# Kernel optimization log

Hardware: AMD Instinct MI355X
Metric: run time of the kernel (lower is better)

Reference implementation:

```python
import jax, jax.numpy as jnp
import numpy as np

B, L, D_MODEL, H = 4, 2048, 1024, 16
HD = D_MODEL // H  # head_dim = 64


def _rope_tables(seq_len, dim, dtype):
    inv_freq = 1.0 / (10000.0 ** (jnp.arange(0, dim, 2, dtype=jnp.float32) / dim))
    t = jnp.arange(seq_len, dtype=jnp.float32)
    freqs = jnp.outer(t, inv_freq)  # (S, dim/2)
    return jnp.cos(freqs).astype(dtype), jnp.sin(freqs).astype(dtype)


def _apply_rope(x):
    # x: (B, H, S, d)
    cos, sin = _rope_tables(x.shape[-2], x.shape[-1], x.dtype)  # (S, d/2)
    x_even = x[..., 0::2]
    x_odd = x[..., 1::2]
    out_even = x_even * cos - x_odd * sin
    out_odd = x_even * sin + x_odd * cos
    return jnp.stack([out_even, out_odd], axis=-1).reshape(x.shape)


def setup_inputs() -> dict:
    key = jax.random.key(0)
    ks = jax.random.split(key, 9)
    s = 1.0 / np.sqrt(D_MODEL)
    inp = {
        "query": jax.random.normal(ks[0], (B, L, D_MODEL), dtype=jnp.float32),
        "Wq": jax.random.uniform(ks[1], (D_MODEL, D_MODEL), jnp.float32, -s, s),
        "bq": jax.random.uniform(ks[2], (D_MODEL,), jnp.float32, -s, s),
        "Wk": jax.random.uniform(ks[3], (D_MODEL, D_MODEL), jnp.float32, -s, s),
        "bk": jax.random.uniform(ks[4], (D_MODEL,), jnp.float32, -s, s),
        "Wv": jax.random.uniform(ks[5], (D_MODEL, D_MODEL), jnp.float32, -s, s),
        "bv": jax.random.uniform(ks[6], (D_MODEL,), jnp.float32, -s, s),
        "Wo": jax.random.uniform(ks[7], (D_MODEL, D_MODEL), jnp.float32, -s, s),
        "bo": jax.random.uniform(ks[8], (D_MODEL,), jnp.float32, -s, s),
    }
    return inp


def reference(query, Wq, bq, Wk, bk, Wv, bv, Wo, bo):
    Bq, Lq, _ = query.shape
    # projections (torch Linear: x @ W.T + b), split into heads -> (B, H, L, d)
    def proj(x, W, b):
        y = x @ W.T + b
        return y.reshape(Bq, Lq, H, HD).transpose(0, 2, 1, 3)
    q = _apply_rope(proj(query, Wq, bq))
    k = _apply_rope(proj(query, Wk, bk))
    v = proj(query, Wv, bv)
    scores = jnp.einsum("bhqd,bhkd->bhqk", q, k) / np.sqrt(HD)
    causal_mask = jnp.triu(jnp.ones((Lq, Lq), dtype=bool), k=1)
    scores = jnp.where(causal_mask[None, None, :, :], -jnp.inf, scores)
    attn = jax.nn.softmax(scores, axis=-1)
    out = jnp.einsum("bhqk,bhkd->bhqd", attn, v)
    out = out.transpose(0, 2, 1, 3).reshape(Bq, Lq, D_MODEL)
    return out @ Wo.T + bo
```

## Files before the change

### kernel.cpp

```cpp
#include <hip/hip_runtime.h>
#include <hip/hip_bf16.h>
#include <math.h>

#define L_SEQ  2048
#define DMODEL 1024
#define NHEAD  16
#define HEADD  64

typedef __attribute__((ext_vector_type(8))) short short8;
typedef __attribute__((ext_vector_type(4))) short short4v;
typedef __attribute__((ext_vector_type(4))) float f32x4;

static __device__ __forceinline__ unsigned short f2bf(float f) {
    unsigned int u = __float_as_uint(f);
    unsigned int r = (u + 0x7fffu + ((u >> 16) & 1u)) >> 16;
    return (unsigned short)r;
}

static __device__ __forceinline__ void dma16(const unsigned short* g, unsigned short* l) {
    __builtin_amdgcn_global_load_lds((const __attribute__((address_space(1))) void*)g,
                                     (__attribute__((address_space(3))) void*)l, 16, 0, 0);
}

__global__ __launch_bounds__(256) void prep(
    const float* __restrict__ query,
    const float* __restrict__ Wq, const float* __restrict__ Wk,
    const float* __restrict__ Wv, const float* __restrict__ Wo,
    unsigned short* __restrict__ xb, unsigned short* __restrict__ wdst,
    float* __restrict__ rope)
{
    int gid = blockIdx.x * 256 + threadIdx.x;
    if (gid < 2097152) {
        float4 v = reinterpret_cast<const float4*>(query)[gid];
        ushort4 o;
        o.x = f2bf(v.x); o.y = f2bf(v.y); o.z = f2bf(v.z); o.w = f2bf(v.w);
        reinterpret_cast<ushort4*>(xb)[gid] = o;
    } else if (gid < 2097152 + 1048576) {
        int i = gid - 2097152;
        int which = i >> 18;
        const float* src = which == 0 ? Wq : which == 1 ? Wk : which == 2 ? Wv : Wo;
        float4 v = reinterpret_cast<const float4*>(src)[i & 262143];
        ushort4 o;
        o.x = f2bf(v.x); o.y = f2bf(v.y); o.z = f2bf(v.z); o.w = f2bf(v.w);
        reinterpret_cast<ushort4*>(wdst)[i] = o;
    } else if (gid < 2097152 + 1048576 + 65536) {
        int i = gid - (2097152 + 1048576);
        int lpos = i >> 5, i2 = i & 31;
        float inv_f = expf(-0.28782313662425574f * (float)i2);
        float ang = (float)lpos * inv_f;
        rope[2 * i]     = cosf(ang);
        rope[2 * i + 1] = sinf(ang);
    }
}

#define BKP 32

__global__ __launch_bounds__(512, 4) void proj_qkv(
    const unsigned short* __restrict__ X,
    const unsigned short* __restrict__ Wqkv,
    const float* __restrict__ bq_,
    const float* __restrict__ bk_,
    const float* __restrict__ bv_,
    const float* __restrict__ rope,
    unsigned short* __restrict__ Qb,
    unsigned short* __restrict__ Kb,
    unsigned short* __restrict__ Vr)
{
    __shared__ unsigned short pool[36864];
    unsigned short* a_ring = pool;
    unsigned short* b_ring = pool + 12288;

    const int tid  = threadIdx.x;
    const int lane = tid & 63;
    const int w    = tid >> 6;
    const int wm   = w & 1, wn = w >> 1;
    const int quad = lane >> 4, l16 = lane & 15;

    const int orig = blockIdx.y * 12 + blockIdx.x;
    const int xcd  = orig & 7;
    const int k    = orig >> 3;
    const int by   = xcd * 8 + (k & 7);
    const int bxp  = k >> 3;
    const int m0   = by * 128;
    const int n0   = bxp * 256;

    const int sel = bxp >> 2;
    const float* bias   = sel == 0 ? bq_ : (sel == 1 ? bk_ : bv_);
    unsigned short* out = sel == 0 ? Qb  : (sel == 1 ? Kb  : Vr);

    const int st_row = lane >> 2;
    const int st_col = (((lane & 3) ^ ((lane >> 3) & 3)) << 3);
    const int rd = ((quad ^ ((l16 >> 1) & 3)) << 3);

    f32x4 acc[4][4];
#pragma unroll
    for (int i = 0; i < 4; ++i)
#pragma unroll
        for (int j = 0; j < 4; ++j) acc[i][j] = (f32x4){0.f, 0.f, 0.f, 0.f};

    const unsigned short* Xs = X    + (size_t)(m0 + w * 16 + st_row) * DMODEL + st_col;
    const unsigned short* Ws = Wqkv + (size_t)(n0 + w * 32 + st_row) * DMODEL + st_col;
    const int ldsA  = (w * 16) * BKP;
    const int ldsB0 = (w * 32) * BKP, ldsB1 = (w * 32 + 16) * BKP;

#pragma unroll
    for (int p = 0; p < 2; ++p) {
        const int kk = p * BKP;
        dma16(Xs + kk,               a_ring + p * 4096 + ldsA);
        dma16(Ws + kk,               b_ring + p * 8192 + ldsB0);
        dma16(Ws + 16 * DMODEL + kk, b_ring + p * 8192 + ldsB1);
    }
    asm volatile("s_waitcnt vmcnt(3)" ::: "memory");
    __builtin_amdgcn_s_barrier();

    for (int kt = 0; kt < 32; ++kt) {
        const int sA = (kt % 3) * 4096;
        const int sB = (kt % 3) * 8192;
        const int pA = ((kt + 2) % 3) * 4096;
        const int pB = ((kt + 2) % 3) * 8192;
        const int kk = ((kt + 2) & 31) * BKP;

        short8 af[4], bf[4];
#pragma unroll
        for (int i = 0; i < 4; ++i)
            af[i] = *reinterpret_cast<const short8*>(
                &a_ring[sA + (wm * 64 + i * 16 + l16) * BKP + rd]);
#pragma unroll
        for (int j = 0; j < 4; ++j)
            bf[j] = *reinterpret_cast<const short8*>(
                &b_ring[sB + (wn * 64 + j * 16 + l16) * BKP + rd]);
        dma16(Xs + kk,               a_ring + pA + ldsA);
        dma16(Ws + kk,               b_ring + pB + ldsB0);
        dma16(Ws + 16 * DMODEL + kk, b_ring + pB + ldsB1);
        __builtin_amdgcn_s_barrier();
        asm volatile("s_waitcnt lgkmcnt(0)" ::: "memory");
        __builtin_amdgcn_sched_barrier(0);
        __builtin_amdgcn_s_setprio(1);
#pragma unroll
        for (int i = 0; i < 4; ++i)
#pragma unroll
            for (int j = 0; j < 4; ++j)
                acc[i][j] = __builtin_amdgcn_mfma_f32_16x16x32_bf16(af[i], bf[j], acc[i][j], 0, 0, 0);
        __builtin_amdgcn_s_setprio(0);
        asm volatile("s_waitcnt vmcnt(3)" ::: "memory");
        __builtin_amdgcn_s_barrier();
    }
    asm volatile("s_waitcnt vmcnt(0)" ::: "memory");
    __builtin_amdgcn_s_barrier();

    const int b     = m0 >> 11;
    const int lpos0 = m0 & (L_SEQ - 1);
#pragma unroll
    for (int t = 0; t < 2; ++t) {
        if ((wn >> 1) == t) {
#pragma unroll
            for (int jf = 0; jf < 4; ++jf) {
                int nl = (wn & 1) * 64 + jf * 16 + l16;
                int nn = (bxp & 3) * 256 + t * 128 + nl;
                float bval = bias[nn];
                int d  = nn & (HEADD - 1);
                float sgn = (d & 1) ? 1.0f : -1.0f;
                int i2 = d >> 1;
#pragma unroll
                for (int mf = 0; mf < 4; ++mf) {
#pragma unroll
                    for (int r = 0; r < 4; ++r) {
                        int ml = wm * 64 + mf * 16 + quad * 4 + r;
                        int lpos = (m0 + ml) & (L_SEQ - 1);
                        float v = acc[mf][jf][r] + bval;
                        if (sel < 2) {
                            float p = __shfl_xor(v, 1);
                            float2 cs = *reinterpret_cast<const float2*>(&rope[(size_t)(lpos * 32 + i2) * 2]);
                            v = v * cs.x + sgn * cs.y * p;
                            if (sel == 0) v *= 0.18033688011112042f;
                        }
                        pool[(sel < 2) ? (ml * 136 + nl) : (nl * 136 + ml)] = f2bf(v);
                    }
                }
            }
        }
        asm volatile("s_waitcnt lgkmcnt(0)" ::: "memory");
        __builtin_amdgcn_s_barrier();
#pragma unroll
        for (int i = 0; i < 4; ++i) {
            int g   = i * 512 + tid;
            int row = g >> 4;
            int c8  = (g & 15) * 8;
            int4 val = *reinterpret_cast<const int4*>(&pool[row * 136 + c8]);
            size_t addr;
            if (sel < 2) {
                int n_g = (bxp & 3) * 256 + t * 128 + c8;
                int h = n_g >> 6, d = n_g & 63;
                addr = ((size_t)(b * NHEAD + h) * L_SEQ + (lpos0 + row)) * HEADD + d;
            } else {
                int n_g = (bxp & 3) * 256 + t * 128 + row;
                int h = n_g >> 6, d = n_g & 63;
                addr = ((size_t)(b * NHEAD + h) * HEADD + d) * L_SEQ + lpos0 + c8;
            }
            *reinterpret_cast<int4*>(out + addr) = val;
        }
        asm volatile("s_waitcnt lgkmcnt(0)" ::: "memory");
        __builtin_amdgcn_s_barrier();
    }
}

__global__ __launch_bounds__(256) void attn_fwd(
    const unsigned short* __restrict__ Q,
    const unsigned short* __restrict__ K,
    const unsigned short* __restrict__ Vt,
    unsigned short* __restrict__ Oa)
{
    __shared__ unsigned short k_lds[2][64 * 64];
    __shared__ unsigned short v_lds[2][64 * 64];
    const int tid  = threadIdx.x;
    const int lane = tid & 63;
    const int w    = tid >> 6;
    const int quad = lane >> 4, l16 = lane & 15;
    const int pair = blockIdx.y;
    const int bh   = blockIdx.x;
    const size_t base = (size_t)bh * L_SEQ * HEADD;
    const int b = bh >> 4, h = bh & 15;

    const int srow  = lane >> 3;
    const int sslot = lane & 7;
    const int ssw   = ((sslot ^ srow) << 3);
    const unsigned short* Ksrc = K  + base + (size_t)(w * 8 + srow) * HEADD + ssw;
    const unsigned short* Vsrc = Vt + base + (size_t)(w * 8 + srow) * L_SEQ + ssw;
    const int d0 = (w * 8) * 64;
    const int d1 = (32 + w * 8) * 64;
    const int swr = (l16 & 7);

    for (int half = 0; half < 2; ++half) {
        const int s = half ? (15 - pair) : pair;
        const int qrow0 = s * 128 + w * 16 + l16;
        const int qrow1 = qrow0 + 64;
        const int kbmax = 2 * s + 1;

        short8 qf0[2], qf1[2];
#pragma unroll
        for (int ks = 0; ks < 2; ++ks) {
            qf0[ks] = *reinterpret_cast<const short8*>(Q + base + (size_t)qrow0 * HEADD + ks * 32 + quad * 8);
            qf1[ks] = *reinterpret_cast<const short8*>(Q + base + (size_t)qrow1 * HEADD + ks * 32 + quad * 8);
        }

        f32x4 o0[4], o1[4];
#pragma unroll
        for (int nt = 0; nt < 4; ++nt) {
            o0[nt] = (f32x4){0.f, 0.f, 0.f, 0.f};
            o1[nt] = (f32x4){0.f, 0.f, 0.f, 0.f};
        }
        float lsum0 = 0.f, lsum1 = 0.f;

        dma16(Ksrc,                 &k_lds[0][d0]);
        dma16(Ksrc + 32 * HEADD,    &k_lds[0][d1]);
        dma16(Vsrc,                 &v_lds[0][d0]);
        dma16(Vsrc + 32 * L_SEQ,    &v_lds[0][d1]);
        asm volatile("s_waitcnt vmcnt(0)" ::: "memory");
        __builtin_amdgcn_s_barrier();

        int cur = 0;
        for (int kb = 0; kb <= kbmax; ++kb) {
            const int kn = (kb + 1) <= kbmax ? (kb + 1) : 0;
            const int nb = cur ^ 1;
            dma16(Ksrc + (size_t)(kn * 64) * HEADD,        &k_lds[nb][d0]);
            dma16(Ksrc + (size_t)(kn * 64 + 32) * HEADD,   &k_lds[nb][d1]);
            dma16(Vsrc + kn * 64,                          &v_lds[nb][d0]);
            dma16(Vsrc + kn * 64 + 32 * L_SEQ,             &v_lds[nb][d1]);

            f32x4 st0[4], st1[4];
#pragma unroll
            for (int nt = 0; nt < 4; ++nt) {
                st0[nt] = (f32x4){0.f, 0.f, 0.f, 0.f};
                st1[nt] = (f32x4){0.f, 0.f, 0.f, 0.f};
            }
            __builtin_amdgcn_s_setprio(1);
#pragma unroll
            for (int ks = 0; ks < 2; ++ks)
#pragma unroll
                for (int nt = 0; nt < 4; ++nt) {
                    short8 kf = *reinterpret_cast<const short8*>(
                        &k_lds[cur][(nt * 16 + l16) * 64 + (((ks * 4 + quad) ^ swr) << 3)]);
                    st0[nt] = __builtin_amdgcn_mfma_f32_16x16x32_bf16(kf, qf0[ks], st0[nt], 0, 0, 0);
                    st1[nt] = __builtin_amdgcn_mfma_f32_16x16x32_bf16(kf, qf1[ks], st1[nt], 0, 0, 0);
                }
            __builtin_amdgcn_s_setprio(0);

            if (kb >= 2 * s) {
#pragma unroll
                for (int nt = 0; nt < 4; ++nt)
#pragma unroll
                    for (int r = 0; r < 4; ++r) {
                        int seqcol = kb * 64 + nt * 16 + quad * 4 + r;
                        if (seqcol > qrow0) st0[nt][r] = -INFINITY;
                    }
            }
            if (kb == kbmax) {
#pragma unroll
                for (int nt = 0; nt < 4; ++nt)
#pragma unroll
                    for (int r = 0; r < 4; ++r) {
                        int seqcol = kb * 64 + nt * 16 + quad * 4 + r;
                        if (seqcol > qrow1) st1[nt][r] = -INFINITY;
                    }
            }

            short4v pfrag0[4], pfrag1[4];
#pragma unroll
            for (int nt = 0; nt < 4; ++nt) {
                float p0 = __builtin_amdgcn_exp2f(st0[nt][0]);
                float p1 = __builtin_amdgcn_exp2f(st0[nt][1]);
                float p2 = __builtin_amdgcn_exp2f(st0[nt][2]);
                float p3 = __builtin_amdgcn_exp2f(st0[nt][3]);
                lsum0 += (p0 + p1) + (p2 + p3);
                unsigned u0 = __float_as_uint(p0) + 0x8000u;
                unsigned u1 = __float_as_uint(p1) + 0x8000u;
                unsigned u2 = __float_as_uint(p2) + 0x8000u;
                unsigned u3 = __float_as_uint(p3) + 0x8000u;
                union { unsigned u[2]; short4v v; } pk;
                pk.u[0] = (u0 >> 16) | (u1 & 0xffff0000u);
                pk.u[1] = (u2 >> 16) | (u3 & 0xffff0000u);
                pfrag0[nt] = pk.v;

                float q0e = __builtin_amdgcn_exp2f(st1[nt][0]);
                float q1e = __builtin_amdgcn_exp2f(st1[nt][1]);
                float q2e = __builtin_amdgcn_exp2f(st1[nt][2]);
                float q3e = __builtin_amdgcn_exp2f(st1[nt][3]);
                lsum1 += (q0e + q1e) + (q2e + q3e);
                unsigned v0 = __float_as_uint(q0e) + 0x8000u;
                unsigned v1 = __float_as_uint(q1e) + 0x8000u;
                unsigned v2 = __float_as_uint(q2e) + 0x8000u;
                unsigned v3 = __float_as_uint(q3e) + 0x8000u;
                union { unsigned u[2]; short4v v; } pk1;
                pk1.u[0] = (v0 >> 16) | (v1 & 0xffff0000u);
                pk1.u[1] = (v2 >> 16) | (v3 & 0xffff0000u);
                pfrag1[nt] = pk1.v;
            }

            __builtin_amdgcn_s_setprio(1);
#pragma unroll
            for (int c = 0; c < 4; ++c)
#pragma unroll
                for (int nt2 = 0; nt2 < 4; ++nt2) {
                    short4v vf = *reinterpret_cast<const short4v*>(
                        &v_lds[cur][(nt2 * 16 + l16) * 64 +
                                    (((c * 2 + (quad >> 1)) ^ swr) << 3) + ((quad & 1) << 2)]);
                    o0[nt2] = __builtin_amdgcn_mfma_f32_16x16x16bf16_1k(pfrag0[c], vf, o0[nt2], 0, 0, 0);
                    o1[nt2] = __builtin_amdgcn_mfma_f32_16x16x16bf16_1k(pfrag1[c], vf, o1[nt2], 0, 0, 0);
                }
            __builtin_amdgcn_s_setprio(0);

            asm volatile("s_waitcnt vmcnt(0)" ::: "memory");
            __builtin_amdgcn_s_barrier();
            cur ^= 1;
        }

        lsum0 += __shfl_xor(lsum0, 16);
        lsum0 += __shfl_xor(lsum0, 32);
        lsum1 += __shfl_xor(lsum1, 16);
        lsum1 += __shfl_xor(lsum1, 32);
        float rs0[4], rs1[4];
#pragma unroll
        for (int r = 0; r < 4; ++r) {
            rs0[r] = __shfl(lsum0, quad * 4 + r);
            rs1[r] = __shfl(lsum1, quad * 4 + r);
        }
#pragma unroll
        for (int r = 0; r < 4; ++r) {
            float inv0 = 1.0f / rs0[r];
            float inv1 = 1.0f / rs1[r];
            int lg0 = s * 128 + w * 16 + quad * 4 + r;
            int lg1 = lg0 + 64;
#pragma unroll
            for (int nt = 0; nt < 4; ++nt) {
                int d = nt * 16 + l16;
                Oa[(size_t)(b * L_SEQ + lg0) * DMODEL + h * HEADD + d] = f2bf(o0[nt][r] * inv0);
                Oa[(size_t)(b * L_SEQ + lg1) * DMODEL + h * HEADD + d] = f2bf(o1[nt][r] * inv1);
            }
        }
    }
}

__global__ __launch_bounds__(256) void out_gemm(
    const unsigned short* __restrict__ X,
    const unsigned short* __restrict__ W,
    const float* __restrict__ bias,
    float* __restrict__ out)
{
    __shared__ unsigned short a_lds[3][128 * BKP];
    __shared__ unsigned short b_lds[3][128 * BKP];
    const int tid  = threadIdx.x;
    const int lane = tid & 63;
    const int w    = tid >> 6;
    const int wm   = w & 1, wn = w >> 1;
    const int quad = lane >> 4, l16 = lane & 15;

    const int orig = blockIdx.y * 8 + blockIdx.x;
    const int xcd  = orig & 7;
    const int k    = orig >> 3;
    const int m0   = (xcd * 8 + (k & 7)) * 128;
    const int n0   = (k >> 3) * 128;

    const int st_row = lane >> 2;
    const int st_col = (((lane & 3) ^ ((lane >> 3) & 3)) << 3);
    const int rd = ((quad ^ ((l16 >> 1) & 3)) << 3);

    f32x4 acc[4][4];
#pragma unroll
    for (int i = 0; i < 4; ++i)
#pragma unroll
        for (int j = 0; j < 4; ++j) acc[i][j] = (f32x4){0.f, 0.f, 0.f, 0.f};

    const unsigned short* Xs = X + (size_t)(m0 + w * 32 + st_row) * DMODEL + st_col;
    const unsigned short* Ws = W + (size_t)(n0 + w * 32 + st_row) * DMODEL + st_col;
    const int ldsA0 = (w * 32) * BKP, ldsA1 = (w * 32 + 16) * BKP;

#pragma unroll
    for (int p = 0; p < 2; ++p) {
        const int kk = p * BKP;
        dma16(Xs + kk,               &a_lds[p][ldsA0]);
        dma16(Xs + 16 * DMODEL + kk, &a_lds[p][ldsA1]);
        dma16(Ws + kk,               &b_lds[p][ldsA0]);
        dma16(Ws + 16 * DMODEL + kk, &b_lds[p][ldsA1]);
    }
    asm volatile("s_waitcnt vmcnt(4)" ::: "memory");
    __builtin_amdgcn_s_barrier();

    for (int kt = 0; kt < 32; ++kt) {
        const int slot = kt % 3;
        const int ps   = (kt + 2) % 3;
        const int kk   = ((kt + 2) & 31) * BKP;

        dma16(Xs + kk,               &a_lds[ps][ldsA0]);
        dma16(Xs + 16 * DMODEL + kk, &a_lds[ps][ldsA1]);
        dma16(Ws + kk,               &b_lds[ps][ldsA0]);
        dma16(Ws + 16 * DMODEL + kk, &b_lds[ps][ldsA1]);

        short8 af[4], bf[4];
#pragma unroll
        for (int i = 0; i < 4; ++i)
            af[i] = *reinterpret_cast<const short8*>(
                &a_lds[slot][(wm * 64 + i * 16 + l16) * BKP + rd]);
#pragma unroll
        for (int j = 0; j < 4; ++j)
            bf[j] = *reinterpret_cast<const short8*>(
                &b_lds[slot][(wn * 64 + j * 16 + l16) * BKP + rd]);
        asm volatile("s_waitcnt lgkmcnt(0)" ::: "memory");
        __builtin_amdgcn_sched_barrier(0);
        __builtin_amdgcn_s_setprio(1);
#pragma unroll
        for (int i = 0; i < 4; ++i)
#pragma unroll
            for (int j = 0; j < 4; ++j)
                acc[i][j] = __builtin_amdgcn_mfma_f32_16x16x32_bf16(af[i], bf[j], acc[i][j], 0, 0, 0);
        __builtin_amdgcn_s_setprio(0);
        asm volatile("s_waitcnt vmcnt(4)" ::: "memory");
        __builtin_amdgcn_s_barrier();
    }
    asm volatile("s_waitcnt vmcnt(0)" ::: "memory");

#pragma unroll
    for (int nt = 0; nt < 4; ++nt) {
        int n_g = n0 + wn * 64 + nt * 16 + l16;
        float bv = bias[n_g];
#pragma unroll
        for (int mt = 0; mt < 4; ++mt)
#pragma unroll
            for (int r = 0; r < 4; ++r) {
                int m_g = m0 + wm * 64 + mt * 16 + quad * 4 + r;
                out[(size_t)m_g * DMODEL + n_g] = acc[mt][nt][r] + bv;
            }
    }
}

extern "C" void kernel_launch(void* const* d_in, const int* in_sizes, int n_in,
                              void* d_out, int out_size, void* d_ws, size_t ws_size,
                              hipStream_t stream) {
    const float* query = (const float*)d_in[0];
    const float* Wq = (const float*)d_in[1];
    const float* bq = (const float*)d_in[2];
    const float* Wk = (const float*)d_in[3];
    const float* bk = (const float*)d_in[4];
    const float* Wv = (const float*)d_in[5];
    const float* bv = (const float*)d_in[6];
    const float* Wo = (const float*)d_in[7];
    const float* bo = (const float*)d_in[8];
    float* out = (float*)d_out;

    unsigned short* ws  = (unsigned short*)d_ws;
    unsigned short* xb  = ws;
    unsigned short* wqb = xb  + (size_t)8388608;
    unsigned short* wkb = wqb + 1048576;
    unsigned short* wvb = wkb + 1048576;
    unsigned short* wob = wvb + 1048576;
    unsigned short* Qb  = wob + 1048576;
    unsigned short* Kb  = Qb  + 8388608;
    unsigned short* Vr  = Kb  + 8388608;
    unsigned short* Ab  = Vr  + 8388608;
    float* rope = (float*)(Ab + 8388608);

    (void)wkb; (void)wvb;

    prep<<<12545, 256, 0, stream>>>(query, Wq, Wk, Wv, Wo, xb, wqb, rope);

    proj_qkv<<<dim3(12, 64), 512, 0, stream>>>(xb, wqb, bq, bk, bv, rope, Qb, Kb, Vr);
    attn_fwd<<<dim3(64, 8), 256, 0, stream>>>(Qb, Kb, Vr, Ab);
    out_gemm<<<dim3(8, 64), 256, 0, stream>>>(Ab, wob, bo, out);
}
```

Before: 277.6 us.

## Triple-buffer K/V tiles in attention with two-block-ahead async prefetch

Expands the K and V LDS staging from double to triple buffering and issues the global-to-LDS DMA two key blocks ahead. The wait becomes vmcnt(4), so only the older block's loads must land before each barrier, letting one block's loads stay in flight across the compute of the next. The goal is to hide global load latency in the attention loop. The cost is 50% more LDS per block, which may lower occupancy, plus modulo-3 slot indexing.

Result: faster. 267.6 us (-3.6%).

```diff
diff --git a/kernel.cpp b/kernel.cpp
--- a/kernel.cpp
+++ b/kernel.cpp
@@ -210,8 +210,8 @@
     const unsigned short* __restrict__ Vt,
     unsigned short* __restrict__ Oa)
 {
-    __shared__ unsigned short k_lds[2][64 * 64];
-    __shared__ unsigned short v_lds[2][64 * 64];
+    __shared__ unsigned short k_lds[3][64 * 64];
+    __shared__ unsigned short v_lds[3][64 * 64];
     const int tid  = threadIdx.x;
     const int lane = tid & 63;
     const int w    = tid >> 6;
@@ -251,21 +251,24 @@
         }
         float lsum0 = 0.f, lsum1 = 0.f;
 
-        dma16(Ksrc,                 &k_lds[0][d0]);
-        dma16(Ksrc + 32 * HEADD,    &k_lds[0][d1]);
-        dma16(Vsrc,                 &v_lds[0][d0]);
-        dma16(Vsrc + 32 * L_SEQ,    &v_lds[0][d1]);
-        asm volatile("s_waitcnt vmcnt(0)" ::: "memory");
-        __builtin_amdgcn_s_barrier();
-
-        int cur = 0;
+#pragma unroll
+        for (int p = 0; p < 2; ++p) {
+            dma16(Ksrc + (size_t)(p * 64) * HEADD,        &k_lds[p][d0]);
+            dma16(Ksrc + (size_t)(p * 64 + 32) * HEADD,   &k_lds[p][d1]);
+            dma16(Vsrc + p * 64,                          &v_lds[p][d0]);
+            dma16(Vsrc + p * 64 + 32 * L_SEQ,             &v_lds[p][d1]);
+        }
+        asm volatile("s_waitcnt vmcnt(4)" ::: "memory");
+        __builtin_amdgcn_s_barrier();
+
         for (int kb = 0; kb <= kbmax; ++kb) {
-            const int kn = (kb + 1) <= kbmax ? (kb + 1) : 0;
-            const int nb = cur ^ 1;
-            dma16(Ksrc + (size_t)(kn * 64) * HEADD,        &k_lds[nb][d0]);
-            dma16(Ksrc + (size_t)(kn * 64 + 32) * HEADD,   &k_lds[nb][d1]);
-            dma16(Vsrc + kn * 64,                          &v_lds[nb][d0]);
-            dma16(Vsrc + kn * 64 + 32 * L_SEQ,             &v_lds[nb][d1]);
+            const int slot = kb % 3;
+            const int ps   = (kb + 2) % 3;
+            const int kn   = (kb + 2) <= kbmax ? (kb + 2) : 0;
+            dma16(Ksrc + (size_t)(kn * 64) * HEADD,        &k_lds[ps][d0]);
+            dma16(Ksrc + (size_t)(kn * 64 + 32) * HEADD,   &k_lds[ps][d1]);
+            dma16(Vsrc + kn * 64,                          &v_lds[ps][d0]);
+            dma16(Vsrc + kn * 64 + 32 * L_SEQ,             &v_lds[ps][d1]);
 
             f32x4 st0[4], st1[4];
 #pragma unroll
@@ -279,7 +282,7 @@
 #pragma unroll
                 for (int nt = 0; nt < 4; ++nt) {
                     short8 kf = *reinterpret_cast<const short8*>(
-                        &k_lds[cur][(nt * 16 + l16) * 64 + (((ks * 4 + quad) ^ swr) << 3)]);
+                        &k_lds[slot][(nt * 16 + l16) * 64 + (((ks * 4 + quad) ^ swr) << 3)]);
                     st0[nt] = __builtin_amdgcn_mfma_f32_16x16x32_bf16(kf, qf0[ks], st0[nt], 0, 0, 0);
                     st1[nt] = __builtin_amdgcn_mfma_f32_16x16x32_bf16(kf, qf1[ks], st1[nt], 0, 0, 0);
                 }
@@ -342,17 +345,18 @@
 #pragma unroll
                 for (int nt2 = 0; nt2 < 4; ++nt2) {
                     short4v vf = *reinterpret_cast<const short4v*>(
-                        &v_lds[cur][(nt2 * 16 + l16) * 64 +
-                                    (((c * 2 + (quad >> 1)) ^ swr) << 3) + ((quad & 1) << 2)]);
+                        &v_lds[slot][(nt2 * 16 + l16) * 64 +
+                                     (((c * 2 + (quad >> 1)) ^ swr) << 3) + ((quad & 1) << 2)]);
                     o0[nt2] = __builtin_amdgcn_mfma_f32_16x16x16bf16_1k(pfrag0[c], vf, o0[nt2], 0, 0, 0);
                     o1[nt2] = __builtin_amdgcn_mfma_f32_16x16x16bf16_1k(pfrag1[c], vf, o1[nt2], 0, 0, 0);
                 }
             __builtin_amdgcn_s_setprio(0);
 
-            asm volatile("s_waitcnt vmcnt(0)" ::: "memory");
+            asm volatile("s_waitcnt vmcnt(4)" ::: "memory");
             __builtin_amdgcn_s_barrier();
-            cur ^= 1;
-        }
+        }
+        asm volatile("s_waitcnt vmcnt(0)" ::: "memory");
+        __builtin_amdgcn_s_barrier();
 
         lsum0 += __shfl_xor(lsum0, 16);
         lsum0 += __shfl_xor(lsum0, 32);
```
